# Performance work log

Hardware: AMD Instinct MI355X
Metric: run time of the kernel (lower is better)

Reference implementation:

```python
import jax, jax.numpy as jnp
import numpy as np

DIM_IN = 1024
DIM_QK = 1024
DIM_V = 1024


def setup_inputs() -> dict:
    key = jax.random.key(0)
    ks = jax.random.split(key, 8)
    s = DIM_IN ** -0.5
    return {
        "x": jax.random.normal(ks[0], (16, 2048, DIM_IN), dtype=jnp.float32),
        "encoder_output": jax.random.normal(ks[1], (16, 2048, DIM_IN), dtype=jnp.float32),
        "W_q": jax.random.normal(ks[2], (DIM_IN, DIM_QK), dtype=jnp.float32) * s,
        "b_q": jnp.zeros((DIM_QK,), dtype=jnp.float32),
        "W_k": jax.random.normal(ks[3], (DIM_IN, DIM_QK), dtype=jnp.float32) * s,
        "b_k": jnp.zeros((DIM_QK,), dtype=jnp.float32),
        "W_v": jax.random.normal(ks[4], (DIM_IN, DIM_V), dtype=jnp.float32) * s,
        "b_v": jnp.zeros((DIM_V,), dtype=jnp.float32),
    }


def reference(x, encoder_output, W_q, b_q, W_k, b_k, W_v, b_v):
    # Q: [B, Lq, Dqk]; K, V: [B, Lk, Dqk/Dv]
    Q = x @ W_q + b_q
    K = encoder_output @ W_k + b_k
    V = encoder_output @ W_v + b_v
    # attn_scores: [B, Lq, Lk], scaled by 1/sqrt(Dqk)
    scores = jnp.einsum("bqd,bkd->bqk", Q, K) * (K.shape[-1] ** -0.5)
    weights = jax.nn.softmax(scores, axis=-1)
    H = jnp.einsum("bqk,bkv->bqv", weights, V)  # [B, Lq, Dv]
    return H
```

## Files before the change

kernel.cpp:

```cpp
#include <hip/hip_runtime.h>

typedef _Float16 f16;
typedef __attribute__((ext_vector_type(4))) _Float16 f16x4;
typedef __attribute__((ext_vector_type(8))) _Float16 f16x8;
typedef __attribute__((ext_vector_type(4))) float f32x4;

#define MFMA16(a, b, c) __builtin_amdgcn_mfma_f32_16x16x32_f16(a, b, c, 0, 0, 0)

__device__ __forceinline__ void gll16(const void* g, void* l) {
    __builtin_amdgcn_global_load_lds(
        (const __attribute__((address_space(1))) unsigned int*)g,
        (__attribute__((address_space(3))) unsigned int*)l, 16, 0, 0);
}

#define BAR() __builtin_amdgcn_s_barrier()
#define LGKM(n) do { asm volatile("s_waitcnt lgkmcnt(" #n ")" ::: "memory"); \
                     __builtin_amdgcn_sched_barrier(0); } while (0)
#define VMC(n)  do { asm volatile("s_waitcnt vmcnt(" #n ")" ::: "memory"); \
                     __builtin_amdgcn_sched_barrier(0); } while (0)

__global__ __launch_bounds__(256) void prep_all(
    const float* __restrict__ x, const float* __restrict__ enc,
    const float* __restrict__ Wq, const float* __restrict__ Wk,
    const float* __restrict__ Wv,
    f16* __restrict__ Xh, f16* __restrict__ Eh, f16* __restrict__ Wt)
{
    const int bid = blockIdx.x;
    if (bid < 32768) {
        const float* in = (bid < 16384) ? x : enc;
        f16* out = (bid < 16384) ? Xh : Eh;
        const int b = bid & 16383;
        const size_t i = ((size_t)b * 256 + threadIdx.x) * 8;
        float4 a = *(const float4*)(in + i);
        float4 c = *(const float4*)(in + i + 4);
        f16x8 o;
        o[0] = (f16)a.x; o[1] = (f16)a.y; o[2] = (f16)a.z; o[3] = (f16)a.w;
        o[4] = (f16)c.x; o[5] = (f16)c.y; o[6] = (f16)c.z; o[7] = (f16)c.w;
        *(f16x8*)(out + i) = o;
        return;
    }
    __shared__ float tile[32][33];
    const int id2 = bid - 32768;
    const int w = id2 >> 10;
    const int r = id2 & 1023;
    const int n0 = (r & 31) * 32, k0 = (r >> 5) * 32;
    const float* W = w == 0 ? Wq : (w == 1 ? Wk : Wv);
    f16* dst = Wt + (size_t)w * 1024 * 1024;
    const int tx = threadIdx.x & 31, ty = threadIdx.x >> 5;
#pragma unroll
    for (int i = 0; i < 4; i++)
        tile[ty + i * 8][tx] = W[(size_t)(k0 + ty + i * 8) * 1024 + n0 + tx];
    __syncthreads();
#pragma unroll
    for (int i = 0; i < 4; i++)
        dst[(size_t)(n0 + ty + i * 8) * 1024 + k0 + tx] = (f16)tile[tx][ty + i * 8];
}

template <int KD, int EPI>
__global__ __launch_bounds__(512, 2) void gemm8(
    const f16* __restrict__ Ab, const f16* __restrict__ Ab2,
    const f16* __restrict__ Bb,
    const float* __restrict__ b0, const float* __restrict__ b1,
    const float* __restrict__ b2, float scale,
    void* __restrict__ C0, void* __restrict__ C1, void* __restrict__ C2,
    float* __restrict__ aux,
    size_t strA, size_t strB, size_t strC, int ldc, int nbx, int nby)
{
    __shared__ f16 shA[2 * 256 * 64];
    __shared__ f16 shB[2 * 256 * 64];

    int id = blockIdx.x;
    {
        const int chunk = (int)gridDim.x >> 3;
        id = (id & 7) * chunk + (id >> 3);
    }
    int bx, by, z;
    bool isQ = false;
    if constexpr (EPI == 4) {
        z = 0;
        isQ = (id < 512);
        if (isQ) { by = id & 3; bx = id >> 2; }
        else     { const int id2 = id - 512; by = id2 & 7; bx = id2 >> 3; }
    } else {
        by = id % nby;
        const int r2 = id / nby;
        bx = r2 % nbx;
        z  = r2 / nbx;
    }
    const int bm = bx * 256, bn = by * 256;

    const f16* A;
    const f16* B;
    if constexpr (EPI == 4) {
        A = isQ ? Ab : Ab2;
        B = Bb + (isQ ? (size_t)0 : (size_t)1024 * 1024);
    } else {
        A = Ab + (size_t)z * strA;
        B = Bb + (size_t)z * strB;
    }

    const int t = threadIdx.x, lane = t & 63, wid = t >> 6;
    const int wr = wid >> 2, wc = wid & 3;
    const int fr = lane & 15, kb = (lane >> 4) * 16;
    const int sw = (fr & 7) << 4;

    const int lsr = lane >> 3;
    const int lsc = ((lane & 7) * 16) ^ (lsr << 4);
    const int a_  = wid * 8;
    const int bq_ = (wid >> 2) * 64 + (wid & 3) * 8;
    const f16* aT0 = A + (size_t)(bm + lsr) * KD + (lsc >> 1) + (size_t)a_ * KD;
    const f16* bT0 = B + (size_t)(bn + lsr) * KD + (lsc >> 1) + (size_t)bq_ * KD;

    const char* Ab_ = (const char*)shA;
    const char* Bb_ = (const char*)shB;
    const int aoffk0 = (wr * 128 + fr) * 128 + (kb ^ sw);
    const int aoffk1 = (wr * 128 + fr) * 128 + ((64 | kb) ^ sw);
    const int boffk0 = (wc * 64 + fr) * 128 + (kb ^ sw);
    const int boffk1 = (wc * 64 + fr) * 128 + ((64 | kb) ^ sw);

#define STG_A0(d, kt) do {                                                    \
        const f16* As_ = aT0 + (size_t)(kt) * 64;                             \
        gll16(As_,                      shA + (d) * 16384 + (a_)*64);         \
        gll16(As_ + (size_t)128 * KD,   shA + (d) * 16384 + (128 + a_)*64); } while (0)
#define STG_A1(d, kt) do {                                                    \
        const f16* As_ = aT0 + (size_t)(kt) * 64;                             \
        gll16(As_ + (size_t)64 * KD,    shA + (d) * 16384 + (64 + a_)*64);    \
        gll16(As_ + (size_t)192 * KD,   shA + (d) * 16384 + (192 + a_)*64); } while (0)
#define STG_B0(d, kt) do {                                                    \
        const f16* Bs_ = bT0 + (size_t)(kt) * 64;                             \
        gll16(Bs_,                      shB + (d) * 16384 + (bq_)*64);        \
        gll16(Bs_ + (size_t)128 * KD,   shB + (d) * 16384 + (128 + bq_)*64); } while (0)
#define STG_B1(d, kt) do {                                                    \
        const f16* Bs_ = bT0 + (size_t)(kt) * 64;                             \
        gll16(Bs_ + (size_t)32 * KD,    shB + (d) * 16384 + (32 + bq_)*64);   \
        gll16(Bs_ + (size_t)160 * KD,   shB + (d) * 16384 + (160 + bq_)*64); } while (0)

    f16x8 af[2][2][4];
    f16x8 bf[2][2][2];
    f32x4 acc[8][4] = {};

#define LDA_(d, mh)                                                           \
    _Pragma("unroll") for (int i_ = 0; i_ < 4; ++i_) {                        \
        af[mh][0][i_] = *(const f16x8*)(Ab_ + (d) * 32768 + aoffk0 +          \
                                        ((mh) * 64 + i_ * 16) * 128);         \
        af[mh][1][i_] = *(const f16x8*)(Ab_ + (d) * 32768 + aoffk1 +          \
                                        ((mh) * 64 + i_ * 16) * 128);         \
    }
#define LDB_(d, nh)                                                           \
    _Pragma("unroll") for (int j_ = 0; j_ < 2; ++j_) {                        \
        bf[nh][0][j_] = *(const f16x8*)(Bb_ + (d) * 32768 + boffk0 +          \
                                        ((nh) * 32 + j_ * 16) * 128);         \
        bf[nh][1][j_] = *(const f16x8*)(Bb_ + (d) * 32768 + boffk1 +          \
                                        ((nh) * 32 + j_ * 16) * 128);         \
    }

#define MM(mh, nh)                                                            \
    __builtin_amdgcn_s_setprio(1);                                            \
    _Pragma("unroll") for (int kk_ = 0; kk_ < 2; ++kk_)                       \
    _Pragma("unroll") for (int i_ = 0; i_ < 4; ++i_)                          \
    _Pragma("unroll") for (int j_ = 0; j_ < 2; ++j_)                          \
        acc[(mh) * 4 + i_][(nh) * 2 + j_] =                                   \
            MFMA16(af[mh][kk_][i_], bf[nh][kk_][j_],                          \
                   acc[(mh) * 4 + i_][(nh) * 2 + j_]);                        \
    __builtin_amdgcn_s_setprio(0);

#define TILE_FULL(d, kt)                                                      \
    do {                                                                      \
        LDA_(d, 0); LDB_(d, 0);                                               \
        STG_A0((d) ^ 1, (kt) + 1); VMC(4);                                    \
        BAR(); LGKM(0); MM(0, 0); BAR();                                      \
        LDB_(d, 1);                                                           \
        STG_B0((d) ^ 1, (kt) + 1); VMC(4);                                    \
        BAR(); LGKM(0); MM(0, 1); BAR();                                      \
        LDA_(d, 1);                                                           \
        STG_B1((d) ^ 1, (kt) + 1);                                            \
        BAR(); LGKM(0); MM(1, 1); BAR();                                      \
        STG_A1((d) ^ 1, (kt) + 1); VMC(4);                                    \
        BAR(); MM(1, 0); BAR();                                               \
    } while (0)

#define TILE_TAIL(d)                                                          \
    do {                                                                      \
        LDA_(d, 0); LDB_(d, 0);                                               \
        VMC(2);                                                               \
        BAR(); LGKM(0); MM(0, 0); BAR();                                      \
        LDB_(d, 1);                                                           \
        VMC(0);                                                               \
        BAR(); LGKM(0); MM(0, 1); BAR();                                      \
        LDA_(d, 1);                                                           \
        BAR(); LGKM(0); MM(1, 1); BAR();                                      \
        BAR(); MM(1, 0); BAR();                                               \
    } while (0)

    constexpr int NT = KD / 64;

    STG_A0(0, 0); STG_B0(0, 0); STG_B1(0, 0); STG_A1(0, 0);
    VMC(4);
    BAR();

    for (int ti = 0; ti < NT - 2; ti += 2) {
        TILE_FULL(0, ti);
        TILE_FULL(1, ti + 1);
    }
    TILE_FULL(0, NT - 2);
    TILE_TAIL(1);

    const int fc = lane & 15, rq = (lane >> 4) * 4;

    if constexpr (EPI == 2) {
        BAR();
        float* part = (float*)shA;
        f16* Sp = (f16*)C0 + (size_t)z * strC;
#pragma unroll
        for (int mi = 0; mi < 8; ++mi)
#pragma unroll
            for (int r = 0; r < 4; ++r) {
                const int rl = wr * 128 + mi * 16 + rq + r;
                float ps = 0.f;
#pragma unroll
                for (int nj = 0; nj < 4; ++nj) {
                    const int col = bn + wc * 64 + nj * 16 + fc;
                    f16 eh = (f16)__expf(acc[mi][nj][r]);
                    ps += (float)eh;
                    Sp[(size_t)(bm + rl) * ldc + col] = eh;
                }
#pragma unroll
                for (int o = 1; o < 16; o <<= 1) ps += __shfl_xor(ps, o);
                if (fc == 0) part[rl * 4 + wc] = ps;
            }
        BAR();
        if (t < 256) {
            const float4 p4 = *(const float4*)(part + t * 4);
            aux[((size_t)z * 2048 + bm + t) * 8 + by] = p4.x + p4.y + p4.z + p4.w;
        }
        return;
    }

    if constexpr (EPI == 5) {
        float invr[8][4];
#pragma unroll
        for (int mi = 0; mi < 8; ++mi)
#pragma unroll
            for (int r = 0; r < 4; ++r) {
                const int row = bm + wr * 128 + mi * 16 + rq + r;
                const float4* p = (const float4*)(aux + ((size_t)z * 2048 + row) * 8);
                const float4 a = p[0], b = p[1];
                invr[mi][r] = 1.0f / (a.x + a.y + a.z + a.w + b.x + b.y + b.z + b.w);
            }
#pragma unroll
        for (int nj = 0; nj < 4; ++nj) {
            const int col = bn + wc * 64 + nj * 16 + fc;
#pragma unroll
            for (int mi = 0; mi < 8; ++mi)
#pragma unroll
                for (int r = 0; r < 4; ++r) {
                    const int row = bm + wr * 128 + mi * 16 + rq + r;
                    ((float*)C0 + (size_t)z * strC)[(size_t)row * ldc + col] =
                        acc[mi][nj][r] * invr[mi][r];
                }
        }
        return;
    }

    if constexpr (EPI == 4) {
#pragma unroll
        for (int nj = 0; nj < 4; ++nj) {
            const int col = bn + wc * 64 + nj * 16 + fc;
            if (isQ) {
                const float bv_ = b0[col];
#pragma unroll
                for (int mi = 0; mi < 8; ++mi)
#pragma unroll
                    for (int r = 0; r < 4; ++r) {
                        const int row = bm + wr * 128 + mi * 16 + rq + r;
                        ((f16*)C0)[(size_t)row * 1024 + col] =
                            (f16)((acc[mi][nj][r] + bv_) * scale);
                    }
            } else {
                const float bv_ = (col < 1024) ? b1[col] : b2[col - 1024];
#pragma unroll
                for (int mi = 0; mi < 8; ++mi) {
                    if (col >= 1024) {
                        const int rowb = bm + wr * 128 + mi * 16 + rq;
                        f16x4 q;
#pragma unroll
                        for (int r = 0; r < 4; ++r) q[r] = (f16)(acc[mi][nj][r] + bv_);
                        f16* Cp = (f16*)C2 + (size_t)(rowb >> 11) * 2048 * 1024 +
                                  (size_t)(col - 1024) * 2048;
                        *(f16x4*)&Cp[rowb & 2047] = q;
                    } else {
#pragma unroll
                        for (int r = 0; r < 4; ++r) {
                            const int row = bm + wr * 128 + mi * 16 + rq + r;
                            ((f16*)C1)[(size_t)row * 1024 + col] =
                                (f16)(acc[mi][nj][r] + bv_);
                        }
                    }
                }
            }
        }
        return;
    }
#undef STG_A0
#undef STG_A1
#undef STG_B0
#undef STG_B1
#undef LDA_
#undef LDB_
#undef MM
#undef TILE_FULL
#undef TILE_TAIL
}

extern "C" void kernel_launch(void* const* d_in, const int* in_sizes, int n_in,
                              void* d_out, int out_size, void* d_ws, size_t ws_size,
                              hipStream_t stream)
{
    const float* x   = (const float*)d_in[0];
    const float* enc = (const float*)d_in[1];
    const float* Wq  = (const float*)d_in[2];
    const float* bq  = (const float*)d_in[3];
    const float* Wk  = (const float*)d_in[4];
    const float* bk  = (const float*)d_in[5];
    const float* Wv  = (const float*)d_in[6];
    const float* bv  = (const float*)d_in[7];

    const size_t TOK = (size_t)16 * 2048;
    f16* Qh = (f16*)d_ws;
    f16* Kh = Qh + TOK * 1024;
    f16* Vt = Kh + TOK * 1024;
    f16* Wt = Vt + TOK * 1024;
    f16* S  = Wt + (size_t)3 * 1024 * 1024;
    f16* Xh = S;
    f16* Eh = S + TOK * 1024;
    float* Ppart = (float*)Wt;

    prep_all<<<35840, 256, 0, stream>>>(x, enc, Wq, Wk, Wv, Xh, Eh, Wt);

    gemm8<1024, 4><<<1536, 512, 0, stream>>>(
        Xh, Eh, Wt, bq, bk, bv, 0.03125f, Qh, Kh, Vt, nullptr,
        0, 0, 0, 1024, 128, 0);

    gemm8<1024, 2><<<1024, 512, 0, stream>>>(
        Qh, nullptr, Kh, nullptr, nullptr, nullptr, 1.0f, S, nullptr, nullptr,
        Ppart,
        (size_t)2048 * 1024, (size_t)2048 * 1024, (size_t)2048 * 2048, 2048, 8, 8);

    gemm8<2048, 5><<<512, 512, 0, stream>>>(
        S, nullptr, Vt, nullptr, nullptr, nullptr, 1.0f, d_out, nullptr, nullptr,
        Ppart,
        (size_t)2048 * 2048, (size_t)1024 * 2048, (size_t)2048 * 1024, 1024, 8, 4);
}
```

Before: 653.9 us.

## Switch GEMM inner loop to 32x32x16 MFMA and precompute row inverses

Replaces the 16x16x32 MFMA tiling with 32x32x16 MFMA instructions. The A/B LDS fragment loads, the accumulator layout and all epilogues are reworked to the 32x32 output mapping, which gives fewer MFMA issues and fewer LDS reads per tile. The softmax normalisation is also changed: a small kernel now reduces the per-row partial sums into reciprocals ahead of time, so the PV GEMM epilogue reads one float per row instead of summing eight partials. This adds a kernel launch and changes the store and shuffle patterns, including a wider 32-lane shuffle reduction in the score epilogue.

```diff
diff --git a/kernel.cpp b/kernel.cpp
--- a/kernel.cpp
+++ b/kernel.cpp
@@ -3,9 +3,9 @@
 typedef _Float16 f16;
 typedef __attribute__((ext_vector_type(4))) _Float16 f16x4;
 typedef __attribute__((ext_vector_type(8))) _Float16 f16x8;
-typedef __attribute__((ext_vector_type(4))) float f32x4;
-
-#define MFMA16(a, b, c) __builtin_amdgcn_mfma_f32_16x16x32_f16(a, b, c, 0, 0, 0)
+typedef __attribute__((ext_vector_type(16))) float f32x16;
+
+#define MFMA32(a, b, c) __builtin_amdgcn_mfma_f32_32x32x16_f16(a, b, c, 0, 0, 0)
 
 __device__ __forceinline__ void gll16(const void* g, void* l) {
     __builtin_amdgcn_global_load_lds(
@@ -101,8 +101,9 @@
 
     const int t = threadIdx.x, lane = t & 63, wid = t >> 6;
     const int wr = wid >> 2, wc = wid & 3;
-    const int fr = lane & 15, kb = (lane >> 4) * 16;
-    const int sw = (fr & 7) << 4;
+    const int fr32 = lane & 31;
+    const int hi   = lane >> 5;
+    const int sw   = (lane & 7) << 4;
 
     const int lsr = lane >> 3;
     const int lsc = ((lane & 7) * 16) ^ (lsr << 4);
@@ -113,10 +114,10 @@
 
     const char* Ab_ = (const char*)shA;
     const char* Bb_ = (const char*)shB;
-    const int aoffk0 = (wr * 128 + fr) * 128 + (kb ^ sw);
-    const int aoffk1 = (wr * 128 + fr) * 128 + ((64 | kb) ^ sw);
-    const int boffk0 = (wc * 64 + fr) * 128 + (kb ^ sw);
-    const int boffk1 = (wc * 64 + fr) * 128 + ((64 | kb) ^ sw);
+    const int ko0 = (hi * 16) ^ sw;
+    const int ko[4] = { ko0, ko0 ^ 32, ko0 ^ 64, ko0 ^ 96 };
+    const int aBase = (wr * 128 + fr32) * 128;
+    const int bBase = (wc * 64 + fr32) * 128;
 
 #define STG_A0(d, kt) do {                                                    \
         const f16* As_ = aT0 + (size_t)(kt) * 64;                             \
@@ -136,32 +137,25 @@
         gll16(Bs_ + (size_t)160 * KD,   shB + (d) * 16384 + (160 + bq_)*64); } while (0)
 
     f16x8 af[2][2][4];
-    f16x8 bf[2][2][2];
-    f32x4 acc[8][4] = {};
+    f16x8 bf[2][4];
+    f32x16 acc[4][2] = {};
 
 #define LDA_(d, mh)                                                           \
-    _Pragma("unroll") for (int i_ = 0; i_ < 4; ++i_) {                        \
-        af[mh][0][i_] = *(const f16x8*)(Ab_ + (d) * 32768 + aoffk0 +          \
-                                        ((mh) * 64 + i_ * 16) * 128);         \
-        af[mh][1][i_] = *(const f16x8*)(Ab_ + (d) * 32768 + aoffk1 +          \
-                                        ((mh) * 64 + i_ * 16) * 128);         \
-    }
+    _Pragma("unroll") for (int m_ = 0; m_ < 2; ++m_)                          \
+    _Pragma("unroll") for (int kc = 0; kc < 4; ++kc)                          \
+        af[mh][m_][kc] = *(const f16x8*)(Ab_ + (d) * 32768 + aBase + ko[kc] + \
+                                         (((mh) * 2 + m_) * 32) * 128);
 #define LDB_(d, nh)                                                           \
-    _Pragma("unroll") for (int j_ = 0; j_ < 2; ++j_) {                        \
-        bf[nh][0][j_] = *(const f16x8*)(Bb_ + (d) * 32768 + boffk0 +          \
-                                        ((nh) * 32 + j_ * 16) * 128);         \
-        bf[nh][1][j_] = *(const f16x8*)(Bb_ + (d) * 32768 + boffk1 +          \
-                                        ((nh) * 32 + j_ * 16) * 128);         \
-    }
+    _Pragma("unroll") for (int kc = 0; kc < 4; ++kc)                          \
+        bf[nh][kc] = *(const f16x8*)(Bb_ + (d) * 32768 + bBase + ko[kc] +     \
+                                     ((nh) * 32) * 128);
 
 #define MM(mh, nh)                                                            \
     __builtin_amdgcn_s_setprio(1);                                            \
-    _Pragma("unroll") for (int kk_ = 0; kk_ < 2; ++kk_)                       \
-    _Pragma("unroll") for (int i_ = 0; i_ < 4; ++i_)                          \
-    _Pragma("unroll") for (int j_ = 0; j_ < 2; ++j_)                          \
-        acc[(mh) * 4 + i_][(nh) * 2 + j_] =                                   \
-            MFMA16(af[mh][kk_][i_], bf[nh][kk_][j_],                          \
-                   acc[(mh) * 4 + i_][(nh) * 2 + j_]);                        \
+    _Pragma("unroll") for (int kc = 0; kc < 4; ++kc)                          \
+    _Pragma("unroll") for (int m_ = 0; m_ < 2; ++m_)                          \
+        acc[(mh) * 2 + m_][nh] =                                              \
+            MFMA32(af[mh][m_][kc], bf[nh][kc], acc[(mh) * 2 + m_][nh]);       \
     __builtin_amdgcn_s_setprio(0);
 
 #define TILE_FULL(d, kt)                                                      \
@@ -205,29 +199,29 @@
     TILE_FULL(0, NT - 2);
     TILE_TAIL(1);
 
-    const int fc = lane & 15, rq = (lane >> 4) * 4;
+    const int col0 = bn + wc * 64 + fr32;
+    const int col1 = col0 + 32;
 
     if constexpr (EPI == 2) {
         BAR();
         float* part = (float*)shA;
         f16* Sp = (f16*)C0 + (size_t)z * strC;
 #pragma unroll
-        for (int mi = 0; mi < 8; ++mi)
-#pragma unroll
-            for (int r = 0; r < 4; ++r) {
-                const int rl = wr * 128 + mi * 16 + rq + r;
-                float ps = 0.f;
-#pragma unroll
-                for (int nj = 0; nj < 4; ++nj) {
-                    const int col = bn + wc * 64 + nj * 16 + fc;
-                    f16 eh = (f16)__expf(acc[mi][nj][r]);
-                    ps += (float)eh;
-                    Sp[(size_t)(bm + rl) * ldc + col] = eh;
+        for (int mt = 0; mt < 4; ++mt)
+#pragma unroll
+            for (int q = 0; q < 4; ++q)
+#pragma unroll
+                for (int j = 0; j < 4; ++j) {
+                    const int rl = wr * 128 + mt * 32 + q * 8 + hi * 4 + j;
+                    f16 h0 = (f16)__expf(acc[mt][0][q * 4 + j]);
+                    f16 h1 = (f16)__expf(acc[mt][1][q * 4 + j]);
+                    Sp[(size_t)(bm + rl) * ldc + col0] = h0;
+                    Sp[(size_t)(bm + rl) * ldc + col1] = h1;
+                    float ps = (float)h0 + (float)h1;
+#pragma unroll
+                    for (int o = 1; o < 32; o <<= 1) ps += __shfl_xor(ps, o);
+                    if (fr32 == 0) part[rl * 4 + wc] = ps;
                 }
-#pragma unroll
-                for (int o = 1; o < 16; o <<= 1) ps += __shfl_xor(ps, o);
-                if (fc == 0) part[rl * 4 + wc] = ps;
-            }
         BAR();
         if (t < 256) {
             const float4 p4 = *(const float4*)(part + t * 4);
@@ -236,68 +230,72 @@
         return;
     }
 
-    if constexpr (EPI == 5) {
-        float invr[8][4];
-#pragma unroll
-        for (int mi = 0; mi < 8; ++mi)
-#pragma unroll
-            for (int r = 0; r < 4; ++r) {
-                const int row = bm + wr * 128 + mi * 16 + rq + r;
-                const float4* p = (const float4*)(aux + ((size_t)z * 2048 + row) * 8);
-                const float4 a = p[0], b = p[1];
-                invr[mi][r] = 1.0f / (a.x + a.y + a.z + a.w + b.x + b.y + b.z + b.w);
-            }
-#pragma unroll
-        for (int nj = 0; nj < 4; ++nj) {
-            const int col = bn + wc * 64 + nj * 16 + fc;
-#pragma unroll
-            for (int mi = 0; mi < 8; ++mi)
-#pragma unroll
-                for (int r = 0; r < 4; ++r) {
-                    const int row = bm + wr * 128 + mi * 16 + rq + r;
-                    ((float*)C0 + (size_t)z * strC)[(size_t)row * ldc + col] =
-                        acc[mi][nj][r] * invr[mi][r];
+    if constexpr (EPI == 3) {
+        float* Cp = (float*)C0 + (size_t)z * strC;
+        const float* Ri = aux + (size_t)z * 2048;
+#pragma unroll
+        for (int mt = 0; mt < 4; ++mt)
+#pragma unroll
+            for (int q = 0; q < 4; ++q)
+#pragma unroll
+                for (int j = 0; j < 4; ++j) {
+                    const int row = bm + wr * 128 + mt * 32 + q * 8 + hi * 4 + j;
+                    const float iv = Ri[row];
+                    Cp[(size_t)row * ldc + col0] = acc[mt][0][q * 4 + j] * iv;
+                    Cp[(size_t)row * ldc + col1] = acc[mt][1][q * 4 + j] * iv;
                 }
-        }
         return;
     }
 
     if constexpr (EPI == 4) {
-#pragma unroll
-        for (int nj = 0; nj < 4; ++nj) {
-            const int col = bn + wc * 64 + nj * 16 + fc;
-            if (isQ) {
-                const float bv_ = b0[col];
-#pragma unroll
-                for (int mi = 0; mi < 8; ++mi)
-#pragma unroll
-                    for (int r = 0; r < 4; ++r) {
-                        const int row = bm + wr * 128 + mi * 16 + rq + r;
-                        ((f16*)C0)[(size_t)row * 1024 + col] =
-                            (f16)((acc[mi][nj][r] + bv_) * scale);
+        if (isQ) {
+            const float bv0 = b0[col0], bv1 = b0[col1];
+#pragma unroll
+            for (int mt = 0; mt < 4; ++mt)
+#pragma unroll
+                for (int q = 0; q < 4; ++q)
+#pragma unroll
+                    for (int j = 0; j < 4; ++j) {
+                        const int row = bm + wr * 128 + mt * 32 + q * 8 + hi * 4 + j;
+                        ((f16*)C0)[(size_t)row * 1024 + col0] =
+                            (f16)((acc[mt][0][q * 4 + j] + bv0) * scale);
+                        ((f16*)C0)[(size_t)row * 1024 + col1] =
+                            (f16)((acc[mt][1][q * 4 + j] + bv1) * scale);
                     }
-            } else {
-                const float bv_ = (col < 1024) ? b1[col] : b2[col - 1024];
-#pragma unroll
-                for (int mi = 0; mi < 8; ++mi) {
-                    if (col >= 1024) {
-                        const int rowb = bm + wr * 128 + mi * 16 + rq;
-                        f16x4 q;
-#pragma unroll
-                        for (int r = 0; r < 4; ++r) q[r] = (f16)(acc[mi][nj][r] + bv_);
-                        f16* Cp = (f16*)C2 + (size_t)(rowb >> 11) * 2048 * 1024 +
-                                  (size_t)(col - 1024) * 2048;
-                        *(f16x4*)&Cp[rowb & 2047] = q;
-                    } else {
-#pragma unroll
-                        for (int r = 0; r < 4; ++r) {
-                            const int row = bm + wr * 128 + mi * 16 + rq + r;
-                            ((f16*)C1)[(size_t)row * 1024 + col] =
-                                (f16)(acc[mi][nj][r] + bv_);
-                        }
+        } else if (bn < 1024) {
+            const float bv0 = b1[col0], bv1 = b1[col1];
+#pragma unroll
+            for (int mt = 0; mt < 4; ++mt)
+#pragma unroll
+                for (int q = 0; q < 4; ++q)
+#pragma unroll
+                    for (int j = 0; j < 4; ++j) {
+                        const int row = bm + wr * 128 + mt * 32 + q * 8 + hi * 4 + j;
+                        ((f16*)C1)[(size_t)row * 1024 + col0] =
+                            (f16)(acc[mt][0][q * 4 + j] + bv0);
+                        ((f16*)C1)[(size_t)row * 1024 + col1] =
+                            (f16)(acc[mt][1][q * 4 + j] + bv1);
                     }
+        } else {
+            const float bv0 = b2[col0 - 1024], bv1 = b2[col1 - 1024];
+#pragma unroll
+            for (int mt = 0; mt < 4; ++mt)
+#pragma unroll
+                for (int q = 0; q < 4; ++q) {
+                    const int rowb = bm + wr * 128 + mt * 32 + q * 8 + hi * 4;
+                    f16x4 q0, q1;
+#pragma unroll
+                    for (int j = 0; j < 4; ++j) {
+                        q0[j] = (f16)(acc[mt][0][q * 4 + j] + bv0);
+                        q1[j] = (f16)(acc[mt][1][q * 4 + j] + bv1);
+                    }
+                    f16* Cp0 = (f16*)C2 + (size_t)(rowb >> 11) * 2048 * 1024 +
+                               (size_t)(col0 - 1024) * 2048;
+                    f16* Cp1 = (f16*)C2 + (size_t)(rowb >> 11) * 2048 * 1024 +
+                               (size_t)(col1 - 1024) * 2048;
+                    *(f16x4*)&Cp0[rowb & 2047] = q0;
+                    *(f16x4*)&Cp1[rowb & 2047] = q1;
                 }
-            }
         }
         return;
     }
@@ -310,6 +308,15 @@
 #undef MM
 #undef TILE_FULL
 #undef TILE_TAIL
+}
+
+__global__ __launch_bounds__(256) void rowinv_k(
+    const float* __restrict__ part, float* __restrict__ inv)
+{
+    const int q = blockIdx.x * 256 + threadIdx.x;
+    const float4* p = (const float4*)(part + (size_t)q * 8);
+    const float4 a = p[0], b = p[1];
+    inv[q] = 1.0f / (a.x + a.y + a.z + a.w + b.x + b.y + b.z + b.w);
 }
 
 extern "C" void kernel_launch(void* const* d_in, const int* in_sizes, int n_in,
@@ -334,6 +341,7 @@
     f16* Xh = S;
     f16* Eh = S + TOK * 1024;
     float* Ppart = (float*)Wt;
+    float* Rinv  = Ppart + TOK * 8;
 
     prep_all<<<35840, 256, 0, stream>>>(x, enc, Wq, Wk, Wv, Xh, Eh, Wt);
 
@@ -346,8 +354,10 @@
         Ppart,
         (size_t)2048 * 1024, (size_t)2048 * 1024, (size_t)2048 * 2048, 2048, 8, 8);
 
-    gemm8<2048, 5><<<512, 512, 0, stream>>>(
+    rowinv_k<<<128, 256, 0, stream>>>(Ppart, Rinv);
+
+    gemm8<2048, 3><<<512, 512, 0, stream>>>(
         S, nullptr, Vt, nullptr, nullptr, nullptr, 1.0f, d_out, nullptr, nullptr,
-        Ppart,
+        Rinv,
         (size_t)2048 * 2048, (size_t)1024 * 2048, (size_t)2048 * 1024, 1024, 8, 4);
 }
```

Result: slower. 675.4 us (+3.3%).
